# Performance work log

Measured on AMD Instinct MI355X. Metric: run time of the kernel, lower is better.

## Reference

```python
import jax, jax.numpy as jnp
import numpy as np

EPS = 1e-8  # torch CosineSimilarity default eps

def _normalize(x):
    # torch clamps each norm at eps before dividing
    n = jnp.sqrt(jnp.sum(x * x, axis=-1, keepdims=True))
    return x / jnp.maximum(n, EPS)

def _cross_entropy(logits, labels):
    logp = jax.nn.log_softmax(logits, axis=-1)
    return -jnp.mean(jnp.take_along_axis(logp, labels[:, None], axis=-1))

def setup_inputs() -> dict:
    key = jax.random.key(0)
    ks = jax.random.split(key, 7)
    B, M, D = 8192, 3129, 512
    return {
        'mm_proj': jax.random.normal(ks[0], (B, D), jnp.float32),
        'ans_embedding': jax.random.normal(ks[1], (M, D), jnp.float32),
        'v_max': jax.random.normal(ks[2], (B, D), jnp.float32),
        'mm': jax.random.normal(ks[3], (B, D), jnp.float32),
        'logits_q': jax.random.normal(ks[4], (B, M), jnp.float32),
        'logits_rubi': jax.random.normal(ks[5], (B, M), jnp.float32),
        'class_id': jax.random.randint(ks[6], (B, 1), 0, M, jnp.int64),
    }

def reference(mm_proj, ans_embedding, v_max, mm, logits_q, logits_rubi, class_id,
              question_loss_weight=1.0):
    cid = class_id.squeeze(1)  # [B]
    # NCE over cosine similarities: fuse normalize + GEMM instead of [B,M,D] expand
    g = _normalize(mm_proj)          # [B, D]
    a = _normalize(ans_embedding)    # [M, D]
    d_logit = jnp.einsum('bd,md->bm', g, a)  # [B, M] cosine matrix
    positive_dist = jnp.take_along_axis(d_logit, cid[:, None], axis=1)[:, 0]  # [B]
    num = jnp.exp(positive_dist)
    den = jnp.sum(jnp.exp(d_logit), axis=-1)
    loss_nce = jnp.mean(-jnp.log(num / den))
    # object cosine loss
    obj_dist = jnp.sum(_normalize(v_max) * _normalize(mm), axis=-1)  # [B]
    obj_loss = jnp.mean(1.0 - obj_dist)
    fusion_loss = (_cross_entropy(logits_rubi, cid) + obj_loss + loss_nce) / 3.0
    question_loss = _cross_entropy(logits_q, cid)
    loss = fusion_loss + question_loss_weight * question_loss
    # out['loss'], out['loss_mm_q'], out['loss_q']
    return jnp.stack([loss, fusion_loss, question_loss])
```

## Files before the change

### kernel.cpp

```cpp
#include <hip/hip_runtime.h>
#include <hip/hip_bf16.h>

#define B_N 8192
#define M_N 3129
#define M_PAD 3200
#define D_N 512

#define CE_L 12
#define CE_SPAN (CE_L * 256)
#define CE_WPA 8344
#define CE_WTOT (2 * CE_WPA)
#define CE_BLOCKS (CE_WTOT / 4)

#define PREP_G_BLOCKS   (B_N / 4)
#define PREP_A_BLOCKS   (M_PAD / 4)
#define PREP_OBJ_BLOCKS (B_N / 4)
#define ZERO_FLOATS (3 * B_N + 8)
#define ZERO_BLOCKS 25
#define A_BLOCKS (PREP_G_BLOCKS + PREP_A_BLOCKS + PREP_OBJ_BLOCKS + ZERO_BLOCKS)

#define GEMM_TILES ((M_PAD / 128) * (B_N / 128))
#define B_BLOCKS 8000

#define GLOBAL_AS __attribute__((address_space(1)))
#define LDS_AS __attribute__((address_space(3)))

typedef __bf16 bf16x8 __attribute__((ext_vector_type(8)));
typedef float f32x4 __attribute__((ext_vector_type(4)));

__device__ __forceinline__ f32x4 nt_load4(const float* p) {
  return __builtin_nontemporal_load((const f32x4*)p);
}

__device__ __forceinline__ void ce_span(
    int gw, const float* __restrict__ lq, const float* __restrict__ lr,
    float* __restrict__ rowsum) {
  const int lane = threadIdx.x & 63;
  const int aidx = (gw >= CE_WPA) ? 1 : 0;
  const unsigned wl = (unsigned)(gw - aidx * CE_WPA);
  const unsigned f0 = wl * (unsigned)CE_SPAN;
  const unsigned r0 = f0 / (unsigned)M_N;
  const unsigned b1 = (r0 + 1u) * (unsigned)M_N;
  const float* base = aidx ? lr : lq;
  const float* p = base + f0 + (unsigned)lane * 4u;

  f32x4 buf[6];
#pragma unroll
  for (int i = 0; i < 6; ++i) buf[i] = nt_load4(p + i * 256);

  float a0 = 0.f, a1 = 0.f;
  const unsigned fbase = f0 + (unsigned)lane * 4u;
#pragma unroll
  for (int i = 0; i < CE_L; ++i) {
    f32x4 v = buf[i % 6];
    if (i + 6 < CE_L) buf[i % 6] = nt_load4(p + (i + 6) * 256);
    unsigned f = fbase + (unsigned)i * 256u;
    float e0 = __expf(v.x), e1 = __expf(v.y), e2 = __expf(v.z), e3 = __expf(v.w);
    float lo = 0.f, hi = 0.f;
    if (f + 0u < b1) lo += e0; else hi += e0;
    if (f + 1u < b1) lo += e1; else hi += e1;
    if (f + 2u < b1) lo += e2; else hi += e2;
    if (f + 3u < b1) lo += e3; else hi += e3;
    a0 += lo; a1 += hi;
  }
  for (int o = 1; o < 64; o <<= 1) {
    a0 += __shfl_xor(a0, o);
    a1 += __shfl_xor(a1, o);
  }
  if (lane == 0) {
    float* rs = rowsum + (aidx ? B_N : 0);
    atomicAdd(rs + r0, a0);
    if (a1 != 0.f) atomicAdd(rs + r0 + 1, a1);
  }
}

__device__ __forceinline__ void normalize_row(
    const float* __restrict__ x, __bf16* __restrict__ y,
    int row, int nrows_src, int lane) {
  bf16x8 out;
  if (row >= nrows_src) {
    for (int j = 0; j < 8; ++j) out[j] = (__bf16)0.0f;
    *(bf16x8*)(y + (size_t)row * D_N + lane * 8) = out;
    return;
  }
  const float* xr = x + (size_t)row * D_N + lane * 8;
  f32x4 v0 = *(const f32x4*)xr;
  f32x4 v1 = *(const f32x4*)(xr + 4);
  float s = v0.x*v0.x + v0.y*v0.y + v0.z*v0.z + v0.w*v0.w
          + v1.x*v1.x + v1.y*v1.y + v1.z*v1.z + v1.w*v1.w;
  for (int o = 1; o < 64; o <<= 1) s += __shfl_xor(s, o);
  float rn = 1.0f / fmaxf(sqrtf(s), 1e-8f);
  float vals[8] = {v0.x, v0.y, v0.z, v0.w, v1.x, v1.y, v1.z, v1.w};
  for (int j = 0; j < 8; ++j) out[j] = (__bf16)(vals[j] * rn);
  *(bf16x8*)(y + (size_t)row * D_N + lane * 8) = out;
}

__global__ __launch_bounds__(256) void a_prep_kernel(
    const float* __restrict__ mm_proj, const float* __restrict__ ans_emb,
    const float* __restrict__ v_max, const float* __restrict__ mm,
    __bf16* __restrict__ g, __bf16* __restrict__ a,
    float* __restrict__ obj, float* __restrict__ zbase) {
  int blk = blockIdx.x;
  int wid = threadIdx.x >> 6, lane = threadIdx.x & 63;
  if (blk < PREP_G_BLOCKS) {
    normalize_row(mm_proj, g, blk * 4 + wid, B_N, lane);
  } else if (blk < PREP_G_BLOCKS + PREP_A_BLOCKS) {
    normalize_row(ans_emb, a, (blk - PREP_G_BLOCKS) * 4 + wid, M_N, lane);
  } else if (blk < PREP_G_BLOCKS + PREP_A_BLOCKS + PREP_OBJ_BLOCKS) {
    int b = (blk - PREP_G_BLOCKS - PREP_A_BLOCKS) * 4 + wid;
    const float* vr = v_max + (size_t)b * D_N + lane * 8;
    const float* mr = mm + (size_t)b * D_N + lane * 8;
    f32x4 a0 = nt_load4(vr), a1 = nt_load4(vr + 4);
    f32x4 b0 = nt_load4(mr), b1 = nt_load4(mr + 4);
    float sv = a0.x*a0.x + a0.y*a0.y + a0.z*a0.z + a0.w*a0.w
             + a1.x*a1.x + a1.y*a1.y + a1.z*a1.z + a1.w*a1.w;
    float sm = b0.x*b0.x + b0.y*b0.y + b0.z*b0.z + b0.w*b0.w
             + b1.x*b1.x + b1.y*b1.y + b1.z*b1.z + b1.w*b1.w;
    float sd = a0.x*b0.x + a0.y*b0.y + a0.z*b0.z + a0.w*b0.w
             + a1.x*b1.x + a1.y*b1.y + a1.z*b1.z + a1.w*b1.w;
    for (int o = 1; o < 64; o <<= 1) {
      sv += __shfl_xor(sv, o);
      sm += __shfl_xor(sm, o);
      sd += __shfl_xor(sd, o);
    }
    if (lane == 0) {
      float dist = sd / (fmaxf(sqrtf(sv), 1e-8f) * fmaxf(sqrtf(sm), 1e-8f));
      obj[b] = 1.0f - dist;
    }
  } else {
    int zb = blk - (PREP_G_BLOCKS + PREP_A_BLOCKS + PREP_OBJ_BLOCKS);
    int idx = (zb * 256 + threadIdx.x) * 4;
    if (idx < ZERO_FLOATS) *(f32x4*)(zbase + idx) = f32x4{0.f, 0.f, 0.f, 0.f};
  }
}

__device__ __forceinline__ void gemm_stage(
    const __bf16* __restrict__ g, const __bf16* __restrict__ a,
    __bf16* As, __bf16* Bs, int t, int brow0, int mrow0, int k0) {
#pragma unroll
  for (int i = 0; i < 2; ++i) {
    int s = t + i * 256;
    int row = s >> 2;
    int kq = (s & 3) << 3;
    const __bf16* ga = g + (size_t)(brow0 + row) * D_N + (k0 + kq);
    __builtin_amdgcn_global_load_lds((const GLOBAL_AS void*)ga,
                                     (LDS_AS void*)(As + s * 8), 16, 0, 0);
    const __bf16* gb = a + (size_t)(mrow0 + row) * D_N + (k0 + kq);
    __builtin_amdgcn_global_load_lds((const GLOBAL_AS void*)gb,
                                     (LDS_AS void*)(Bs + s * 8), 16, 0, 0);
  }
}

__global__ __launch_bounds__(256) void b_fused_kernel(
    const __bf16* __restrict__ g, const __bf16* __restrict__ a,
    const int* __restrict__ cid,
    const float* __restrict__ lq, const float* __restrict__ lr,
    float* __restrict__ den, float* __restrict__ pos,
    float* __restrict__ rowsum) {
  __shared__ __bf16 As[2][128 * 32];
  __shared__ __bf16 Bs[2][128 * 32];
  const int t = threadIdx.x;
  const int lane = t & 63;
  const int wid = t >> 6;
  const int blk = blockIdx.x;
  const int mod = blk % 5;
  const int d5 = blk / 5;

  if (mod == 2) {
    const int xcd = blk & 7;
    const int tile = xcd * (GEMM_TILES / 8) + (d5 >> 3);
    const int brow0 = (tile / (M_PAD / 128)) * 128;
    const int mrow0 = (tile % (M_PAD / 128)) * 128;
    const int wrow = wid >> 1;
    const int wcol = wid & 1;
    const int r = lane & 15;
    const int quad = lane >> 4;

    f32x4 acc[4][4];
    for (int i = 0; i < 4; ++i)
      for (int j = 0; j < 4; ++j)
        acc[i][j] = f32x4{0.f, 0.f, 0.f, 0.f};

    gemm_stage(g, a, &As[0][0], &Bs[0][0], t, brow0, mrow0, 0);
    int cur = 0;
    __syncthreads();

    for (int ks = 0; ks < D_N / 32; ++ks) {
      if (ks + 1 < D_N / 32)
        gemm_stage(g, a, &As[cur ^ 1][0], &Bs[cur ^ 1][0], t, brow0, mrow0,
                   (ks + 1) * 32);
      bf16x8 af[4], bfr[4];
#pragma unroll
      for (int i = 0; i < 4; ++i)
        af[i] = *(const bf16x8*)(&As[cur][(wrow * 64 + i * 16 + r) * 32 + quad * 8]);
#pragma unroll
      for (int j = 0; j < 4; ++j)
        bfr[j] = *(const bf16x8*)(&Bs[cur][(wcol * 64 + j * 16 + r) * 32 + quad * 8]);
#pragma unroll
      for (int i = 0; i < 4; ++i)
#pragma unroll
        for (int j = 0; j < 4; ++j)
          acc[i][j] = __builtin_amdgcn_mfma_f32_16x16x32_bf16(af[i], bfr[j],
                                                              acc[i][j], 0, 0, 0);
      __syncthreads();
      cur ^= 1;
    }

    for (int i = 0; i < 4; ++i) {
      for (int reg = 0; reg < 4; ++reg) {
        int b = brow0 + wrow * 64 + i * 16 + quad * 4 + reg;
        int lab = cid[b];
        float s = 0.0f;
#pragma unroll
        for (int j = 0; j < 4; ++j) {
          int m = mrow0 + wcol * 64 + j * 16 + r;
          float v = acc[i][j][reg];
          if (m < M_N) s += __expf(v);
          if (m == lab) pos[b] = v;
        }
        s += __shfl_xor(s, 1);
        s += __shfl_xor(s, 2);
        s += __shfl_xor(s, 4);
        s += __shfl_xor(s, 8);
        if (r == 0) atomicAdd(den + b, s);
      }
    }
    return;
  }

  const int other = d5 * 4 + mod - (mod > 2 ? 1 : 0);
  const int om = other % 3;
  if (om != 2) {
    const int ce_idx = (other / 3) * 2 + om;
    if (ce_idx < CE_BLOCKS) ce_span(ce_idx * 4 + wid, lq, lr, rowsum);
  }
}

__global__ __launch_bounds__(256) void c_final_kernel(
    const float* __restrict__ den, const float* __restrict__ pos,
    const float* __restrict__ rowsum,
    const float* __restrict__ lq, const float* __restrict__ lr,
    const int* __restrict__ cid, const float* __restrict__ obj,
    float* __restrict__ acc, float* __restrict__ out) {
  int b = blockIdx.x * 256 + threadIdx.x;
  int lab = cid[b];
  float xq = lq[(size_t)b * M_N + lab];
  float xr = lr[(size_t)b * M_N + lab];
  float s_nce = logf(den[b]) - pos[b];
  float s_ceq = logf(rowsum[b]) - xq;
  float s_cer = logf(rowsum[B_N + b]) - xr;
  float s_obj = obj[b];
  for (int o = 1; o < 64; o <<= 1) {
    s_nce += __shfl_xor(s_nce, o);
    s_ceq += __shfl_xor(s_ceq, o);
    s_cer += __shfl_xor(s_cer, o);
    s_obj += __shfl_xor(s_obj, o);
  }
  __shared__ float red[4][4];
  int wid = threadIdx.x >> 6;
  if ((threadIdx.x & 63) == 0) {
    red[wid][0] = s_nce; red[wid][1] = s_ceq;
    red[wid][2] = s_cer; red[wid][3] = s_obj;
  }
  __syncthreads();
  if (threadIdx.x < 4) {
    float v = red[0][threadIdx.x] + red[1][threadIdx.x]
            + red[2][threadIdx.x] + red[3][threadIdx.x];
    atomicAdd(acc + threadIdx.x, v);
  }
  if (threadIdx.x == 0) {
    __threadfence();
    unsigned prev = atomicAdd((unsigned*)(acc + 4), 1u);
    if (prev == 31u) {
      float nce = atomicAdd(acc + 0, 0.0f) / (float)B_N;
      float ceq = atomicAdd(acc + 1, 0.0f) / (float)B_N;
      float cer = atomicAdd(acc + 2, 0.0f) / (float)B_N;
      float ob  = atomicAdd(acc + 3, 0.0f) / (float)B_N;
      float fusion = (cer + ob + nce) * (1.0f / 3.0f);
      out[0] = fusion + ceq;
      out[1] = fusion;
      out[2] = ceq;
    }
  }
}

extern "C" void kernel_launch(void* const* d_in, const int* in_sizes, int n_in,
                              void* d_out, int out_size, void* d_ws, size_t ws_size,
                              hipStream_t stream) {
  const float* mm_proj     = (const float*)d_in[0];
  const float* ans_emb     = (const float*)d_in[1];
  const float* v_max       = (const float*)d_in[2];
  const float* mm          = (const float*)d_in[3];
  const float* logits_q    = (const float*)d_in[4];
  const float* logits_rubi = (const float*)d_in[5];
  const int*   cid         = (const int*)d_in[6];
  float* out = (float*)d_out;

  char* ws = (char*)d_ws;
  __bf16* g = (__bf16*)ws;
  __bf16* a = (__bf16*)(ws + 8388608);
  float* den    = (float*)(ws + 8388608 + 3276800);
  float* rowsum = den + B_N;
  float* acc    = rowsum + 2 * B_N;
  float* pos    = acc + 8;
  float* obj    = pos + B_N;

  a_prep_kernel<<<A_BLOCKS, 256, 0, stream>>>(
      mm_proj, ans_emb, v_max, mm, g, a, obj, den);
  b_fused_kernel<<<B_BLOCKS, 256, 0, stream>>>(
      g, a, cid, logits_q, logits_rubi, den, pos, rowsum);
  c_final_kernel<<<B_N / 256, 256, 0, stream>>>(
      den, pos, rowsum, logits_q, logits_rubi, cid, obj, acc, out);
}
```

Before: 303.2 us.

## Move object cosine loss into fused kernel and reorder block schedule

Moves the v_max/mm cosine-distance work out of the prep kernel and into the fused GEMM/cross-entropy kernel as extra trailing blocks. The interleaved 1-in-5 GEMM block schedule becomes a contiguous order: all GEMM tiles first, then the cross-entropy spans, then the object blocks. The aim is to shorten the prep kernel on the critical path and let the memory-bound object and CE streams overlap with the GEMM tail. The risk is that grouping GEMM tiles first removes the earlier compute/memory interleaving, and the grid size must still cover all the new work.

```diff
diff --git a/kernel.cpp b/kernel.cpp
--- a/kernel.cpp
+++ b/kernel.cpp
@@ -14,13 +14,13 @@
 
 #define PREP_G_BLOCKS   (B_N / 4)
 #define PREP_A_BLOCKS   (M_PAD / 4)
-#define PREP_OBJ_BLOCKS (B_N / 4)
 #define ZERO_FLOATS (3 * B_N + 8)
 #define ZERO_BLOCKS 25
-#define A_BLOCKS (PREP_G_BLOCKS + PREP_A_BLOCKS + PREP_OBJ_BLOCKS + ZERO_BLOCKS)
+#define A_BLOCKS (PREP_G_BLOCKS + PREP_A_BLOCKS + ZERO_BLOCKS)
 
 #define GEMM_TILES ((M_PAD / 128) * (B_N / 128))
 #define B_BLOCKS 8000
+#define OBJ_BLOCKS (B_N / 4)
 
 #define GLOBAL_AS __attribute__((address_space(1)))
 #define LDS_AS __attribute__((address_space(3)))
@@ -97,17 +97,122 @@
 
 __global__ __launch_bounds__(256) void a_prep_kernel(
     const float* __restrict__ mm_proj, const float* __restrict__ ans_emb,
-    const float* __restrict__ v_max, const float* __restrict__ mm,
     __bf16* __restrict__ g, __bf16* __restrict__ a,
-    float* __restrict__ obj, float* __restrict__ zbase) {
+    float* __restrict__ zbase) {
   int blk = blockIdx.x;
   int wid = threadIdx.x >> 6, lane = threadIdx.x & 63;
   if (blk < PREP_G_BLOCKS) {
     normalize_row(mm_proj, g, blk * 4 + wid, B_N, lane);
   } else if (blk < PREP_G_BLOCKS + PREP_A_BLOCKS) {
     normalize_row(ans_emb, a, (blk - PREP_G_BLOCKS) * 4 + wid, M_N, lane);
-  } else if (blk < PREP_G_BLOCKS + PREP_A_BLOCKS + PREP_OBJ_BLOCKS) {
-    int b = (blk - PREP_G_BLOCKS - PREP_A_BLOCKS) * 4 + wid;
+  } else {
+    int zb = blk - (PREP_G_BLOCKS + PREP_A_BLOCKS);
+    int idx = (zb * 256 + threadIdx.x) * 4;
+    if (idx < ZERO_FLOATS) *(f32x4*)(zbase + idx) = f32x4{0.f, 0.f, 0.f, 0.f};
+  }
+}
+
+__device__ __forceinline__ void gemm_stage(
+    const __bf16* __restrict__ g, const __bf16* __restrict__ a,
+    __bf16* As, __bf16* Bs, int t, int brow0, int mrow0, int k0) {
+#pragma unroll
+  for (int i = 0; i < 2; ++i) {
+    int s = t + i * 256;
+    int row = s >> 2;
+    int kq = (s & 3) << 3;
+    const __bf16* ga = g + (size_t)(brow0 + row) * D_N + (k0 + kq);
+    __builtin_amdgcn_global_load_lds((const GLOBAL_AS void*)ga,
+                                     (LDS_AS void*)(As + s * 8), 16, 0, 0);
+    const __bf16* gb = a + (size_t)(mrow0 + row) * D_N + (k0 + kq);
+    __builtin_amdgcn_global_load_lds((const GLOBAL_AS void*)gb,
+                                     (LDS_AS void*)(Bs + s * 8), 16, 0, 0);
+  }
+}
+
+__global__ __launch_bounds__(256) void b_fused_kernel(
+    const __bf16* __restrict__ g, const __bf16* __restrict__ a,
+    const int* __restrict__ cid,
+    const float* __restrict__ v_max, const float* __restrict__ mm,
+    const float* __restrict__ lq, const float* __restrict__ lr,
+    float* __restrict__ den, float* __restrict__ pos,
+    float* __restrict__ rowsum, float* __restrict__ obj) {
+  __shared__ __bf16 As[2][128 * 32];
+  __shared__ __bf16 Bs[2][128 * 32];
+  const int t = threadIdx.x;
+  const int lane = t & 63;
+  const int wid = t >> 6;
+  const int blk = blockIdx.x;
+
+  if (blk < GEMM_TILES) {
+    const int xcd = blk & 7;
+    const int tile = xcd * (GEMM_TILES / 8) + (blk >> 3);
+    const int brow0 = (tile / (M_PAD / 128)) * 128;
+    const int mrow0 = (tile % (M_PAD / 128)) * 128;
+    const int wrow = wid >> 1;
+    const int wcol = wid & 1;
+    const int r = lane & 15;
+    const int quad = lane >> 4;
+
+    f32x4 acc[4][4];
+    for (int i = 0; i < 4; ++i)
+      for (int j = 0; j < 4; ++j)
+        acc[i][j] = f32x4{0.f, 0.f, 0.f, 0.f};
+
+    gemm_stage(g, a, &As[0][0], &Bs[0][0], t, brow0, mrow0, 0);
+    int cur = 0;
+    __syncthreads();
+
+    for (int ks = 0; ks < D_N / 32; ++ks) {
+      if (ks + 1 < D_N / 32)
+        gemm_stage(g, a, &As[cur ^ 1][0], &Bs[cur ^ 1][0], t, brow0, mrow0,
+                   (ks + 1) * 32);
+      bf16x8 af[4], bfr[4];
+#pragma unroll
+      for (int i = 0; i < 4; ++i)
+        af[i] = *(const bf16x8*)(&As[cur][(wrow * 64 + i * 16 + r) * 32 + quad * 8]);
+#pragma unroll
+      for (int j = 0; j < 4; ++j)
+        bfr[j] = *(const bf16x8*)(&Bs[cur][(wcol * 64 + j * 16 + r) * 32 + quad * 8]);
+#pragma unroll
+      for (int i = 0; i < 4; ++i)
+#pragma unroll
+        for (int j = 0; j < 4; ++j)
+          acc[i][j] = __builtin_amdgcn_mfma_f32_16x16x32_bf16(af[i], bfr[j],
+                                                              acc[i][j], 0, 0, 0);
+      __syncthreads();
+      cur ^= 1;
+    }
+
+    for (int i = 0; i < 4; ++i) {
+      for (int reg = 0; reg < 4; ++reg) {
+        int b = brow0 + wrow * 64 + i * 16 + quad * 4 + reg;
+        int lab = cid[b];
+        float s = 0.0f;
+#pragma unroll
+        for (int j = 0; j < 4; ++j) {
+          int m = mrow0 + wcol * 64 + j * 16 + r;
+          float v = acc[i][j][reg];
+          if (m < M_N) s += __expf(v);
+          if (m == lab) pos[b] = v;
+        }
+        s += __shfl_xor(s, 1);
+        s += __shfl_xor(s, 2);
+        s += __shfl_xor(s, 4);
+        s += __shfl_xor(s, 8);
+        if (r == 0) atomicAdd(den + b, s);
+      }
+    }
+    return;
+  }
+
+  const int ord = blk - GEMM_TILES;
+  if (ord < CE_BLOCKS) {
+    ce_span(ord * 4 + wid, lq, lr, rowsum);
+    return;
+  }
+  const int oo = ord - CE_BLOCKS;
+  if (oo < OBJ_BLOCKS) {
+    int b = oo * 4 + wid;
     const float* vr = v_max + (size_t)b * D_N + lane * 8;
     const float* mr = mm + (size_t)b * D_N + lane * 8;
     f32x4 a0 = nt_load4(vr), a1 = nt_load4(vr + 4);
@@ -127,112 +232,6 @@
       float dist = sd / (fmaxf(sqrtf(sv), 1e-8f) * fmaxf(sqrtf(sm), 1e-8f));
       obj[b] = 1.0f - dist;
     }
-  } else {
-    int zb = blk - (PREP_G_BLOCKS + PREP_A_BLOCKS + PREP_OBJ_BLOCKS);
-    int idx = (zb * 256 + threadIdx.x) * 4;
-    if (idx < ZERO_FLOATS) *(f32x4*)(zbase + idx) = f32x4{0.f, 0.f, 0.f, 0.f};
-  }
-}
-
-__device__ __forceinline__ void gemm_stage(
-    const __bf16* __restrict__ g, const __bf16* __restrict__ a,
-    __bf16* As, __bf16* Bs, int t, int brow0, int mrow0, int k0) {
-#pragma unroll
-  for (int i = 0; i < 2; ++i) {
-    int s = t + i * 256;
-    int row = s >> 2;
-    int kq = (s & 3) << 3;
-    const __bf16* ga = g + (size_t)(brow0 + row) * D_N + (k0 + kq);
-    __builtin_amdgcn_global_load_lds((const GLOBAL_AS void*)ga,
-                                     (LDS_AS void*)(As + s * 8), 16, 0, 0);
-    const __bf16* gb = a + (size_t)(mrow0 + row) * D_N + (k0 + kq);
-    __builtin_amdgcn_global_load_lds((const GLOBAL_AS void*)gb,
-                                     (LDS_AS void*)(Bs + s * 8), 16, 0, 0);
-  }
-}
-
-__global__ __launch_bounds__(256) void b_fused_kernel(
-    const __bf16* __restrict__ g, const __bf16* __restrict__ a,
-    const int* __restrict__ cid,
-    const float* __restrict__ lq, const float* __restrict__ lr,
-    float* __restrict__ den, float* __restrict__ pos,
-    float* __restrict__ rowsum) {
-  __shared__ __bf16 As[2][128 * 32];
-  __shared__ __bf16 Bs[2][128 * 32];
-  const int t = threadIdx.x;
-  const int lane = t & 63;
-  const int wid = t >> 6;
-  const int blk = blockIdx.x;
-  const int mod = blk % 5;
-  const int d5 = blk / 5;
-
-  if (mod == 2) {
-    const int xcd = blk & 7;
-    const int tile = xcd * (GEMM_TILES / 8) + (d5 >> 3);
-    const int brow0 = (tile / (M_PAD / 128)) * 128;
-    const int mrow0 = (tile % (M_PAD / 128)) * 128;
-    const int wrow = wid >> 1;
-    const int wcol = wid & 1;
-    const int r = lane & 15;
-    const int quad = lane >> 4;
-
-    f32x4 acc[4][4];
-    for (int i = 0; i < 4; ++i)
-      for (int j = 0; j < 4; ++j)
-        acc[i][j] = f32x4{0.f, 0.f, 0.f, 0.f};
-
-    gemm_stage(g, a, &As[0][0], &Bs[0][0], t, brow0, mrow0, 0);
-    int cur = 0;
-    __syncthreads();
-
-    for (int ks = 0; ks < D_N / 32; ++ks) {
-      if (ks + 1 < D_N / 32)
-        gemm_stage(g, a, &As[cur ^ 1][0], &Bs[cur ^ 1][0], t, brow0, mrow0,
-                   (ks + 1) * 32);
-      bf16x8 af[4], bfr[4];
-#pragma unroll
-      for (int i = 0; i < 4; ++i)
-        af[i] = *(const bf16x8*)(&As[cur][(wrow * 64 + i * 16 + r) * 32 + quad * 8]);
-#pragma unroll
-      for (int j = 0; j < 4; ++j)
-        bfr[j] = *(const bf16x8*)(&Bs[cur][(wcol * 64 + j * 16 + r) * 32 + quad * 8]);
-#pragma unroll
-      for (int i = 0; i < 4; ++i)
-#pragma unroll
-        for (int j = 0; j < 4; ++j)
-          acc[i][j] = __builtin_amdgcn_mfma_f32_16x16x32_bf16(af[i], bfr[j],
-                                                              acc[i][j], 0, 0, 0);
-      __syncthreads();
-      cur ^= 1;
-    }
-
-    for (int i = 0; i < 4; ++i) {
-      for (int reg = 0; reg < 4; ++reg) {
-        int b = brow0 + wrow * 64 + i * 16 + quad * 4 + reg;
-        int lab = cid[b];
-        float s = 0.0f;
-#pragma unroll
-        for (int j = 0; j < 4; ++j) {
-          int m = mrow0 + wcol * 64 + j * 16 + r;
-          float v = acc[i][j][reg];
-          if (m < M_N) s += __expf(v);
-          if (m == lab) pos[b] = v;
-        }
-        s += __shfl_xor(s, 1);
-        s += __shfl_xor(s, 2);
-        s += __shfl_xor(s, 4);
-        s += __shfl_xor(s, 8);
-        if (r == 0) atomicAdd(den + b, s);
-      }
-    }
-    return;
-  }
-
-  const int other = d5 * 4 + mod - (mod > 2 ? 1 : 0);
-  const int om = other % 3;
-  if (om != 2) {
-    const int ce_idx = (other / 3) * 2 + om;
-    if (ce_idx < CE_BLOCKS) ce_span(ce_idx * 4 + wid, lq, lr, rowsum);
   }
 }
 
@@ -305,10 +304,9 @@
   float* pos    = acc + 8;
   float* obj    = pos + B_N;
 
-  a_prep_kernel<<<A_BLOCKS, 256, 0, stream>>>(
-      mm_proj, ans_emb, v_max, mm, g, a, obj, den);
+  a_prep_kernel<<<A_BLOCKS, 256, 0, stream>>>(mm_proj, ans_emb, g, a, den);
   b_fused_kernel<<<B_BLOCKS, 256, 0, stream>>>(
-      g, a, cid, logits_q, logits_rubi, den, pos, rowsum);
+      g, a, cid, v_max, mm, logits_q, logits_rubi, den, pos, rowsum, obj);
   c_final_kernel<<<B_N / 256, 256, 0, stream>>>(
       den, pos, rowsum, logits_q, logits_rubi, cid, obj, acc, out);
 }
```

Measured after the change: 300.2 us. No clear change (-1.0%).
